# Kernel tuning notes

Measured on AMD Instinct MI355X. Metric: run time of the kernel, lower is better.

## Reference

```python
import jax, jax.numpy as jnp
import numpy as np

B, T, D, H = 32, 4096, 512, 512


def setup_inputs() -> dict:
    key = jax.random.key(0)
    ks = jax.random.split(key, 8)
    s = 1.0 / np.sqrt(D)
    return {
        "hidden_state": jax.random.normal(ks[0], (B, D), jnp.float32),
        "encoder_outputs": jax.random.normal(ks[1], (B, T, D), jnp.float32),
        "W": jax.random.normal(ks[2], (D, H), jnp.float32) * s,
        "U": jax.random.normal(ks[3], (D, H), jnp.float32) * s,
        "V": jax.random.normal(ks[4], (H,), jnp.float32) * s,
        "bias": jnp.zeros((H,), jnp.float32),
        "Wa": jax.random.normal(ks[5], (H, H), jnp.float32) * (1.0 / np.sqrt(H)),
        "ba": jnp.zeros((H,), jnp.float32),
    }


def reference(hidden_state, encoder_outputs, W, U, V, bias, Wa, ba):
    # dens1: [B,1,H] ; dens2: [B,T,H]
    dens1 = jnp.einsum('bd,dh->bh', hidden_state, W)[:, None, :]
    dens2 = jnp.einsum('btd,dh->bth', encoder_outputs, U)
    pre = dens1 + dens2 + bias                       # [B,T,H]
    tanh_ = jnp.tanh(jnp.einsum('bth,hk->btk', pre, Wa) + ba)  # extra Dense(tanh)
    cij = jnp.einsum('bth,h->bt', tanh_, V)          # [B,T]
    alphas = jax.nn.softmax(cij, axis=-1)            # [B,T]
    output = jnp.einsum('btd,bt->bd', encoder_outputs, alphas)  # weighted sum
    return output, alphas
```

## Files before the change

### kernel.cpp

```cpp
#include <hip/hip_runtime.h>
#include <hip/hip_bf16.h>


#define BB 32
#define TT 4096
#define DD 512
#define HH 512

typedef short s16x8 __attribute__((ext_vector_type(8)));
typedef float f32x4 __attribute__((ext_vector_type(4)));

union FU { float f; unsigned u; };

static __device__ __forceinline__ unsigned pack_bf16_trunc(float a, float b) {
    FU ua, ub; ua.f = a; ub.f = b;
    return (ua.u >> 16) | (ub.u & 0xffff0000u);
}

static __device__ __forceinline__ unsigned short f2bf_rne(float x) {
    FU v; v.f = x;
    unsigned u = v.u;
    u = u + 0x7fffu + ((u >> 16) & 1u);
    return (unsigned short)(u >> 16);
}

static __device__ __forceinline__ float tanh_fast(float x) {
    float e = __expf(2.0f * x);
    return 1.0f - 2.0f * __builtin_amdgcn_rcpf(e + 1.0f);
}

__global__ void k_prep(const float* __restrict__ hs, const float* __restrict__ W,
                       const float* __restrict__ bias, const float* __restrict__ Wa,
                       const float* __restrict__ ba, const float* __restrict__ U,
                       float* __restrict__ cvec, unsigned short* __restrict__ Btf) {
    int bi = blockIdx.x;
    int tid = threadIdx.x;
    __shared__ float sm[8 * DD];
    if (bi < 32) {
        int b = bi;
        float* hsb = sm;
        float* gs = sm + DD;
        hsb[tid] = hs[b * DD + tid];
        hsb[tid + 256] = hs[b * DD + tid + 256];
        __syncthreads();
        float a0 = bias[tid], a1 = bias[tid + 256];
        #pragma unroll 4
        for (int d = 0; d < DD; ++d) {
            float h = hsb[d];
            a0 = fmaf(h, W[(size_t)d * HH + tid], a0);
            a1 = fmaf(h, W[(size_t)d * HH + tid + 256], a1);
        }
        gs[tid] = a0;
        gs[tid + 256] = a1;
        __syncthreads();
        float c0 = ba[tid], c1 = ba[tid + 256];
        #pragma unroll 4
        for (int h = 0; h < HH; ++h) {
            float g = gs[h];
            c0 = fmaf(g, Wa[(size_t)h * HH + tid], c0);
            c1 = fmaf(g, Wa[(size_t)h * HH + tid + 256], c1);
        }
        cvec[b * HH + tid] = c0;
        cvec[b * HH + tid + 256] = c1;
    } else {
        int d0 = (bi - 32) * 8;
        float (*Us)[DD] = (float (*)[DD])sm;
        #pragma unroll
        for (int i = 0; i < 16; ++i) {
            int idx = i * 256 + tid;
            Us[idx >> 9][idx & 511] = U[(size_t)(d0 + (idx >> 9)) * HH + (idx & 511)];
        }
        __syncthreads();
        float acc[8][2] = {};
        #pragma unroll 2
        for (int h = 0; h < DD; ++h) {
            float w0 = Wa[(size_t)h * HH + tid];
            float w1 = Wa[(size_t)h * HH + 256 + tid];
            #pragma unroll
            for (int dd = 0; dd < 8; ++dd) {
                float u = Us[dd][h];
                acc[dd][0] = fmaf(u, w0, acc[dd][0]);
                acc[dd][1] = fmaf(u, w1, acc[dd][1]);
            }
        }
        int fk = d0 >> 5, qq = (d0 >> 3) & 3;
        #pragma unroll
        for (int half = 0; half < 2; ++half) {
            int n = tid + half * 256;
            unsigned short tmp[8];
            #pragma unroll
            for (int dd = 0; dd < 8; ++dd) tmp[dd] = f2bf_rne(acc[dd][half]);
            size_t base = ((size_t)((n >> 4) * 16 + fk) * 64 + (n & 15) + (qq << 4)) * 8;
            *(uint4*)&Btf[base] = *(const uint4*)tmp;
        }
    }
}

__global__ void __launch_bounds__(256, 2) k_gemm_tanh(
    const float* __restrict__ e, const unsigned short* __restrict__ Btf,
    const float* __restrict__ cvec, const float* __restrict__ V,
    float* __restrict__ cij) {
    int tid = threadIdx.x;
    int m0 = blockIdx.x * 64;
    int lane = tid & 63, w = tid >> 6;
    int wn = w * 128;
    int lcol = lane & 15, q = lane >> 4;

    __shared__ __align__(16) unsigned short As[64 * DD];

    const float* Abase = e + (size_t)m0 * DD;
    #pragma unroll
    for (int it = 0; it < 16; ++it) {
        int idx = it * 256 + tid;
        int m = idx >> 6, c2 = idx & 63;
        const float* p = Abase + (size_t)m * DD + c2 * 8;
        float4 v0 = *(const float4*)p;
        float4 v1 = *(const float4*)(p + 4);
        uint4 u;
        u.x = pack_bf16_trunc(v0.x, v0.y);
        u.y = pack_bf16_trunc(v0.z, v0.w);
        u.z = pack_bf16_trunc(v1.x, v1.y);
        u.w = pack_bf16_trunc(v1.z, v1.w);
        *(uint4*)&As[(m * 64 + (c2 ^ m)) * 8] = u;
    }
    __syncthreads();

    const unsigned short* Bw = Btf + (size_t)(w * 8) * 16 * 64 * 8;
    f32x4 acc[4][8] = {};
    s16x8 bfr[2][8];
    #pragma unroll
    for (int j = 0; j < 8; ++j)
        bfr[0][j] = *(const s16x8*)(Bw + ((size_t)(j * 16 + 0) * 64 + lane) * 8);

    #pragma unroll
    for (int kk = 0; kk < 16; ++kk) {
        int cur = kk & 1;
        if (kk < 15) {
            #pragma unroll
            for (int j = 0; j < 8; ++j)
                bfr[cur ^ 1][j] =
                    *(const s16x8*)(Bw + ((size_t)(j * 16 + kk + 1) * 64 + lane) * 8);
        }
        s16x8 af[4];
        #pragma unroll
        for (int i = 0; i < 4; ++i) {
            int m = i * 16 + lcol;
            af[i] = *(const s16x8*)&As[(m * 64 + ((kk * 4 + q) ^ m)) * 8];
        }
        #pragma unroll
        for (int i = 0; i < 4; ++i)
            #pragma unroll
            for (int j = 0; j < 8; ++j)
                acc[i][j] = __builtin_amdgcn_mfma_f32_16x16x32_bf16(
                    af[i], bfr[cur][j], acc[i][j], 0, 0, 0);
    }

    __syncthreads();
    float* red = (float*)As;
    int b = m0 >> 12;
    float cvv[8], Vv[8];
    #pragma unroll
    for (int j = 0; j < 8; ++j) {
        int h = wn + j * 16 + lcol;
        cvv[j] = cvec[b * HH + h];
        Vv[j] = V[h];
    }
    #pragma unroll
    for (int i = 0; i < 4; ++i) {
        #pragma unroll
        for (int r = 0; r < 4; ++r) {
            float s = 0.0f;
            #pragma unroll
            for (int j = 0; j < 8; ++j)
                s = fmaf(tanh_fast(acc[i][j][r] + cvv[j]), Vv[j], s);
            s += __shfl_xor(s, 1);
            s += __shfl_xor(s, 2);
            s += __shfl_xor(s, 4);
            s += __shfl_xor(s, 8);
            if (lcol == 0)
                red[w * 64 + i * 16 + q * 4 + r] = s;
        }
    }
    __syncthreads();
    if (tid < 64)
        cij[m0 + tid] = red[tid] + red[64 + tid] + red[128 + tid] + red[192 + tid];
}

__global__ void k_softmax(const float* __restrict__ cij, float* __restrict__ alphas) {
    int b = blockIdx.x, tid = threadIdx.x;
    const float* row = cij + (size_t)b * TT;
    __shared__ float red[4];
    float m = -1e30f;
    for (int t = tid; t < TT; t += 256) m = fmaxf(m, row[t]);
    #pragma unroll
    for (int o = 1; o < 64; o <<= 1) m = fmaxf(m, __shfl_xor(m, o));
    if ((tid & 63) == 0) red[tid >> 6] = m;
    __syncthreads();
    m = fmaxf(fmaxf(red[0], red[1]), fmaxf(red[2], red[3]));
    __syncthreads();
    float sum = 0.0f;
    for (int t = tid; t < TT; t += 256) sum += __expf(row[t] - m);
    #pragma unroll
    for (int o = 1; o < 64; o <<= 1) sum += __shfl_xor(sum, o);
    if ((tid & 63) == 0) red[tid >> 6] = sum;
    __syncthreads();
    float inv = 1.0f / (red[0] + red[1] + red[2] + red[3]);
    for (int t = tid; t < TT; t += 256)
        alphas[(size_t)b * TT + t] = __expf(row[t] - m) * inv;
}

__global__ void k_wsum(const float* __restrict__ e, const float* __restrict__ alphas,
                       float* __restrict__ pw) {
    int b = blockIdx.x >> 6;
    int chunk = blockIdx.x & 63;
    int tid = threadIdx.x;
    int half = tid >> 7, f4 = tid & 127;
    const float* base = e + (size_t)b * TT * DD + (size_t)chunk * 64 * DD + f4 * 4;
    const float* al = alphas + (size_t)b * TT + chunk * 64;
    f32x4 a0 = {0,0,0,0}, a1 = {0,0,0,0}, a2 = {0,0,0,0}, a3 = {0,0,0,0};
    for (int it = 0; it < 8; ++it) {
        int t = it * 8 + half;
        float w0 = al[t], w1 = al[t + 2], w2 = al[t + 4], w3 = al[t + 6];
        a0 += w0 * *(const f32x4*)(base + (size_t)t * DD);
        a1 += w1 * *(const f32x4*)(base + (size_t)(t + 2) * DD);
        a2 += w2 * *(const f32x4*)(base + (size_t)(t + 4) * DD);
        a3 += w3 * *(const f32x4*)(base + (size_t)(t + 6) * DD);
    }
    a0 += a1; a2 += a3; a0 += a2;
    __shared__ f32x4 red[128];
    if (half == 1) red[f4] = a0;
    __syncthreads();
    if (half == 0) {
        a0 += red[f4];
        *(f32x4*)&pw[((size_t)(b * 64 + chunk)) * DD + f4 * 4] = a0;
    }
}

__global__ void k_wred(const float* __restrict__ pw, float* __restrict__ out) {
    int b = blockIdx.x, tid = threadIdx.x;
    float2 acc = {0.0f, 0.0f};
    const float* base = pw + (size_t)b * 64 * DD;
    #pragma unroll 4
    for (int c = 0; c < 64; ++c) {
        float2 v = *(const float2*)(base + (size_t)c * DD + tid * 2);
        acc.x += v.x;
        acc.y += v.y;
    }
    *(float2*)&out[b * DD + tid * 2] = acc;
}

extern "C" void kernel_launch(void* const* d_in, const int* in_sizes, int n_in,
                              void* d_out, int out_size, void* d_ws, size_t ws_size,
                              hipStream_t stream) {
    const float* hs   = (const float*)d_in[0];
    const float* e    = (const float*)d_in[1];
    const float* W    = (const float*)d_in[2];
    const float* U    = (const float*)d_in[3];
    const float* V    = (const float*)d_in[4];
    const float* bias = (const float*)d_in[5];
    const float* Wa   = (const float*)d_in[6];
    const float* ba   = (const float*)d_in[7];

    float* out    = (float*)d_out;
    float* alphas = out + BB * DD;

    float*          cij  = (float*)d_ws;
    float*          cvec = (float*)((char*)d_ws + 524288);
    unsigned short* Btf  = (unsigned short*)((char*)d_ws + 589824);
    float*          pw   = (float*)((char*)d_ws + 1179648);


    k_prep<<<96, 256, 0, stream>>>(hs, W, bias, Wa, ba, U, cvec, Btf);
    k_gemm_tanh<<<2048, 256, 0, stream>>>(e, Btf, cvec, V, cij);
    k_softmax<<<BB, 256, 0, stream>>>(cij, alphas);
    k_wsum<<<BB * 64, 256, 0, stream>>>(e, alphas, pw);
    k_wred<<<BB, 256, 0, stream>>>(pw, out);
}
```

Measured before the change: 574.3 us.

## Split GEMM-tanh across two N-halves with K-staged shared memory and partial scores

The fused GEMM+tanh kernel now launches twice as many blocks, each covering half of the H columns. The A tile is staged through shared memory in two K halves, cutting shared memory and accumulator registers so occupancy can rise (launch bounds 2→3). Each N-half writes its own partial score, and softmax sums the two and caches the exponentials in shared memory so they are not recomputed. In exchange, every encoder row is now read and converted to bf16 twice, and the kernel adds an extra sync and a larger workspace.

```diff
diff --git a/kernel.cpp b/kernel.cpp
--- a/kernel.cpp
+++ b/kernel.cpp
@@ -96,72 +96,76 @@
     }
 }
 
-__global__ void __launch_bounds__(256, 2) k_gemm_tanh(
+__global__ void __launch_bounds__(256, 3) k_gemm_tanh(
     const float* __restrict__ e, const unsigned short* __restrict__ Btf,
     const float* __restrict__ cvec, const float* __restrict__ V,
-    float* __restrict__ cij) {
+    float* __restrict__ cijp) {
     int tid = threadIdx.x;
-    int m0 = blockIdx.x * 64;
+    int nh = blockIdx.x & 1;
+    int m0 = (blockIdx.x >> 1) * 64;
     int lane = tid & 63, w = tid >> 6;
-    int wn = w * 128;
     int lcol = lane & 15, q = lane >> 4;
 
-    __shared__ __align__(16) unsigned short As[64 * DD];
+    __shared__ __align__(16) unsigned short As[64 * 256];
 
     const float* Abase = e + (size_t)m0 * DD;
-    #pragma unroll
-    for (int it = 0; it < 16; ++it) {
-        int idx = it * 256 + tid;
-        int m = idx >> 6, c2 = idx & 63;
-        const float* p = Abase + (size_t)m * DD + c2 * 8;
-        float4 v0 = *(const float4*)p;
-        float4 v1 = *(const float4*)(p + 4);
-        uint4 u;
-        u.x = pack_bf16_trunc(v0.x, v0.y);
-        u.y = pack_bf16_trunc(v0.z, v0.w);
-        u.z = pack_bf16_trunc(v1.x, v1.y);
-        u.w = pack_bf16_trunc(v1.z, v1.w);
-        *(uint4*)&As[(m * 64 + (c2 ^ m)) * 8] = u;
-    }
-    __syncthreads();
-
-    const unsigned short* Bw = Btf + (size_t)(w * 8) * 16 * 64 * 8;
-    f32x4 acc[4][8] = {};
-    s16x8 bfr[2][8];
-    #pragma unroll
-    for (int j = 0; j < 8; ++j)
-        bfr[0][j] = *(const s16x8*)(Bw + ((size_t)(j * 16 + 0) * 64 + lane) * 8);
-
-    #pragma unroll
-    for (int kk = 0; kk < 16; ++kk) {
-        int cur = kk & 1;
-        if (kk < 15) {
-            #pragma unroll
-            for (int j = 0; j < 8; ++j)
-                bfr[cur ^ 1][j] =
-                    *(const s16x8*)(Bw + ((size_t)(j * 16 + kk + 1) * 64 + lane) * 8);
-        }
-        s16x8 af[4];
-        #pragma unroll
-        for (int i = 0; i < 4; ++i) {
-            int m = i * 16 + lcol;
-            af[i] = *(const s16x8*)&As[(m * 64 + ((kk * 4 + q) ^ m)) * 8];
-        }
-        #pragma unroll
-        for (int i = 0; i < 4; ++i)
-            #pragma unroll
-            for (int j = 0; j < 8; ++j)
-                acc[i][j] = __builtin_amdgcn_mfma_f32_16x16x32_bf16(
-                    af[i], bfr[cur][j], acc[i][j], 0, 0, 0);
+    f32x4 acc[4][4] = {};
+    s16x8 bfr[2][4];
+    const unsigned short* Bw = Btf + (size_t)(nh * 16 + w * 4) * 16 * 64 * 8;
+
+    #pragma unroll
+    for (int half = 0; half < 2; ++half) {
+        if (half) __syncthreads();
+        #pragma unroll 2
+        for (int it = 0; it < 8; ++it) {
+            int idx = it * 256 + tid;
+            int m = idx >> 5, c2 = idx & 31;
+            const float* p = Abase + (size_t)m * DD + half * 256 + c2 * 8;
+            float4 v0 = *(const float4*)p;
+            float4 v1 = *(const float4*)(p + 4);
+            uint4 u;
+            u.x = pack_bf16_trunc(v0.x, v0.y);
+            u.y = pack_bf16_trunc(v0.z, v0.w);
+            u.z = pack_bf16_trunc(v1.x, v1.y);
+            u.w = pack_bf16_trunc(v1.z, v1.w);
+            *(uint4*)&As[(m * 32 + (c2 ^ (m & 31))) * 8] = u;
+        }
+        __syncthreads();
+        #pragma unroll
+        for (int j = 0; j < 4; ++j)
+            bfr[0][j] = *(const s16x8*)(Bw +
+                ((size_t)(j * 16 + half * 8) * 64 + lane) * 8);
+        #pragma unroll
+        for (int kk = 0; kk < 8; ++kk) {
+            int cur = kk & 1;
+            if (kk < 7) {
+                #pragma unroll
+                for (int j = 0; j < 4; ++j)
+                    bfr[cur ^ 1][j] = *(const s16x8*)(Bw +
+                        ((size_t)(j * 16 + half * 8 + kk + 1) * 64 + lane) * 8);
+            }
+            s16x8 af[4];
+            #pragma unroll
+            for (int i = 0; i < 4; ++i) {
+                int m = i * 16 + lcol;
+                af[i] = *(const s16x8*)&As[(m * 32 + ((kk * 4 + q) ^ (m & 31))) * 8];
+            }
+            #pragma unroll
+            for (int i = 0; i < 4; ++i)
+                #pragma unroll
+                for (int j = 0; j < 4; ++j)
+                    acc[i][j] = __builtin_amdgcn_mfma_f32_16x16x32_bf16(
+                        af[i], bfr[cur][j], acc[i][j], 0, 0, 0);
+        }
     }
 
     __syncthreads();
     float* red = (float*)As;
     int b = m0 >> 12;
-    float cvv[8], Vv[8];
-    #pragma unroll
-    for (int j = 0; j < 8; ++j) {
-        int h = wn + j * 16 + lcol;
+    float cvv[4], Vv[4];
+    #pragma unroll
+    for (int j = 0; j < 4; ++j) {
+        int h = nh * 256 + w * 64 + j * 16 + lcol;
         cvv[j] = cvec[b * HH + h];
         Vv[j] = V[h];
     }
@@ -171,7 +175,7 @@
         for (int r = 0; r < 4; ++r) {
             float s = 0.0f;
             #pragma unroll
-            for (int j = 0; j < 8; ++j)
+            for (int j = 0; j < 4; ++j)
                 s = fmaf(tanh_fast(acc[i][j][r] + cvv[j]), Vv[j], s);
             s += __shfl_xor(s, 1);
             s += __shfl_xor(s, 2);
@@ -183,15 +187,18 @@
     }
     __syncthreads();
     if (tid < 64)
-        cij[m0 + tid] = red[tid] + red[64 + tid] + red[128 + tid] + red[192 + tid];
-}
-
-__global__ void k_softmax(const float* __restrict__ cij, float* __restrict__ alphas) {
+        cijp[(size_t)nh * (BB * TT) + m0 + tid] =
+            red[tid] + red[64 + tid] + red[128 + tid] + red[192 + tid];
+}
+
+__global__ void k_softmax(const float* __restrict__ cijp, float* __restrict__ alphas) {
     int b = blockIdx.x, tid = threadIdx.x;
-    const float* row = cij + (size_t)b * TT;
+    const float* r0 = cijp + (size_t)b * TT;
+    const float* r1 = r0 + (size_t)BB * TT;
     __shared__ float red[4];
+    __shared__ float rowbuf[TT / 256 * 256];
     float m = -1e30f;
-    for (int t = tid; t < TT; t += 256) m = fmaxf(m, row[t]);
+    for (int t = tid; t < TT; t += 256) m = fmaxf(m, r0[t] + r1[t]);
     #pragma unroll
     for (int o = 1; o < 64; o <<= 1) m = fmaxf(m, __shfl_xor(m, o));
     if ((tid & 63) == 0) red[tid >> 6] = m;
@@ -199,14 +206,18 @@
     m = fmaxf(fmaxf(red[0], red[1]), fmaxf(red[2], red[3]));
     __syncthreads();
     float sum = 0.0f;
-    for (int t = tid; t < TT; t += 256) sum += __expf(row[t] - m);
+    for (int t = tid; t < TT; t += 256) {
+        float v = __expf(r0[t] + r1[t] - m);
+        rowbuf[t & 4095] = v;
+        sum += v;
+    }
     #pragma unroll
     for (int o = 1; o < 64; o <<= 1) sum += __shfl_xor(sum, o);
     if ((tid & 63) == 0) red[tid >> 6] = sum;
     __syncthreads();
     float inv = 1.0f / (red[0] + red[1] + red[2] + red[3]);
     for (int t = tid; t < TT; t += 256)
-        alphas[(size_t)b * TT + t] = __expf(row[t] - m) * inv;
+        alphas[(size_t)b * TT + t] = rowbuf[t] * inv;
 }
 
 __global__ void k_wsum(const float* __restrict__ e, const float* __restrict__ alphas,
@@ -264,15 +275,15 @@
     float* out    = (float*)d_out;
     float* alphas = out + BB * DD;
 
-    float*          cij  = (float*)d_ws;
-    float*          cvec = (float*)((char*)d_ws + 524288);
-    unsigned short* Btf  = (unsigned short*)((char*)d_ws + 589824);
-    float*          pw   = (float*)((char*)d_ws + 1179648);
+    float*          cijp = (float*)d_ws;
+    float*          cvec = (float*)((char*)d_ws + 1048576);
+    unsigned short* Btf  = (unsigned short*)((char*)d_ws + 1114112);
+    float*          pw   = (float*)((char*)d_ws + 1703936);
 
 
     k_prep<<<96, 256, 0, stream>>>(hs, W, bias, Wa, ba, U, cvec, Btf);
-    k_gemm_tanh<<<2048, 256, 0, stream>>>(e, Btf, cvec, V, cij);
-    k_softmax<<<BB, 256, 0, stream>>>(cij, alphas);
+    k_gemm_tanh<<<4096, 256, 0, stream>>>(e, Btf, cvec, V, cijp);
+    k_softmax<<<BB, 256, 0, stream>>>(cijp, alphas);
     k_wsum<<<BB * 64, 256, 0, stream>>>(e, alphas, pw);
     k_wred<<<BB, 256, 0, stream>>>(pw, out);
 }
```

New measurement: 577.9 us. About the same (+0.6%).

## Shrink GEMM M-tile to 32 rows with 8 waves, cache softmax exps in LDS

Applied to the files above, without the earlier changes.

The fused GEMM+tanh kernel now handles 32 rows per block with 512 threads (8 waves, each owning 64 output columns), halving per-wave accumulators and LDS so more blocks fit per CU. The A-tile swizzle is reworked for the smaller tile, and the cross-wave reduction is extended to sum 8 partials. Softmax stores exp values in shared memory so they are not recomputed, and the weighted-sum loop gets an unroll hint. The trade-off is that each B fragment loaded from global/L2 is reused across half as many rows, which doubles total B traffic.

```diff
diff --git a/kernel.cpp b/kernel.cpp
--- a/kernel.cpp
+++ b/kernel.cpp
@@ -96,22 +96,21 @@
     }
 }
 
-__global__ void __launch_bounds__(256, 2) k_gemm_tanh(
+__global__ void __launch_bounds__(512, 4) k_gemm_tanh(
     const float* __restrict__ e, const unsigned short* __restrict__ Btf,
     const float* __restrict__ cvec, const float* __restrict__ V,
     float* __restrict__ cij) {
     int tid = threadIdx.x;
-    int m0 = blockIdx.x * 64;
+    int m0 = blockIdx.x * 32;
     int lane = tid & 63, w = tid >> 6;
-    int wn = w * 128;
     int lcol = lane & 15, q = lane >> 4;
 
-    __shared__ __align__(16) unsigned short As[64 * DD];
+    __shared__ __align__(16) unsigned short As[32 * 512];
 
     const float* Abase = e + (size_t)m0 * DD;
     #pragma unroll
-    for (int it = 0; it < 16; ++it) {
-        int idx = it * 256 + tid;
+    for (int it = 0; it < 4; ++it) {
+        int idx = it * 512 + tid;
         int m = idx >> 6, c2 = idx & 63;
         const float* p = Abase + (size_t)m * DD + c2 * 8;
         float4 v0 = *(const float4*)p;
@@ -121,36 +120,38 @@
         u.y = pack_bf16_trunc(v0.z, v0.w);
         u.z = pack_bf16_trunc(v1.x, v1.y);
         u.w = pack_bf16_trunc(v1.z, v1.w);
-        *(uint4*)&As[(m * 64 + (c2 ^ m)) * 8] = u;
-    }
-    __syncthreads();
-
-    const unsigned short* Bw = Btf + (size_t)(w * 8) * 16 * 64 * 8;
-    f32x4 acc[4][8] = {};
-    s16x8 bfr[2][8];
-    #pragma unroll
-    for (int j = 0; j < 8; ++j)
-        bfr[0][j] = *(const s16x8*)(Bw + ((size_t)(j * 16 + 0) * 64 + lane) * 8);
+        *(uint4*)&As[(m * 64 + (c2 >> 5) * 32 + ((c2 & 31) ^ (m & 31))) * 8] = u;
+    }
+    __syncthreads();
+
+    const unsigned short* Bw = Btf + (size_t)(w * 4) * 16 * 64 * 8;
+    f32x4 acc[2][4] = {};
+    s16x8 bfr[2][4];
+    #pragma unroll
+    for (int j = 0; j < 4; ++j)
+        bfr[0][j] = *(const s16x8*)(Bw + ((size_t)(j * 16) * 64 + lane) * 8);
 
     #pragma unroll
     for (int kk = 0; kk < 16; ++kk) {
         int cur = kk & 1;
         if (kk < 15) {
             #pragma unroll
-            for (int j = 0; j < 8; ++j)
-                bfr[cur ^ 1][j] =
-                    *(const s16x8*)(Bw + ((size_t)(j * 16 + kk + 1) * 64 + lane) * 8);
-        }
-        s16x8 af[4];
-        #pragma unroll
-        for (int i = 0; i < 4; ++i) {
+            for (int j = 0; j < 4; ++j)
+                bfr[cur ^ 1][j] = *(const s16x8*)(Bw +
+                    ((size_t)(j * 16 + kk + 1) * 64 + lane) * 8);
+        }
+        s16x8 af[2];
+        #pragma unroll
+        for (int i = 0; i < 2; ++i) {
             int m = i * 16 + lcol;
-            af[i] = *(const s16x8*)&As[(m * 64 + ((kk * 4 + q) ^ m)) * 8];
-        }
-        #pragma unroll
-        for (int i = 0; i < 4; ++i)
-            #pragma unroll
-            for (int j = 0; j < 8; ++j)
+            int c2 = kk * 4 + q;
+            af[i] = *(const s16x8*)&As[
+                (m * 64 + (c2 >> 5) * 32 + ((c2 & 31) ^ (m & 31))) * 8];
+        }
+        #pragma unroll
+        for (int i = 0; i < 2; ++i)
+            #pragma unroll
+            for (int j = 0; j < 4; ++j)
                 acc[i][j] = __builtin_amdgcn_mfma_f32_16x16x32_bf16(
                     af[i], bfr[cur][j], acc[i][j], 0, 0, 0);
     }
@@ -158,38 +159,43 @@
     __syncthreads();
     float* red = (float*)As;
     int b = m0 >> 12;
-    float cvv[8], Vv[8];
-    #pragma unroll
-    for (int j = 0; j < 8; ++j) {
-        int h = wn + j * 16 + lcol;
+    float cvv[4], Vv[4];
+    #pragma unroll
+    for (int j = 0; j < 4; ++j) {
+        int h = w * 64 + j * 16 + lcol;
         cvv[j] = cvec[b * HH + h];
         Vv[j] = V[h];
     }
     #pragma unroll
-    for (int i = 0; i < 4; ++i) {
+    for (int i = 0; i < 2; ++i) {
         #pragma unroll
         for (int r = 0; r < 4; ++r) {
             float s = 0.0f;
             #pragma unroll
-            for (int j = 0; j < 8; ++j)
+            for (int j = 0; j < 4; ++j)
                 s = fmaf(tanh_fast(acc[i][j][r] + cvv[j]), Vv[j], s);
             s += __shfl_xor(s, 1);
             s += __shfl_xor(s, 2);
             s += __shfl_xor(s, 4);
             s += __shfl_xor(s, 8);
             if (lcol == 0)
-                red[w * 64 + i * 16 + q * 4 + r] = s;
-        }
-    }
-    __syncthreads();
-    if (tid < 64)
-        cij[m0 + tid] = red[tid] + red[64 + tid] + red[128 + tid] + red[192 + tid];
+                red[w * 32 + i * 16 + q * 4 + r] = s;
+        }
+    }
+    __syncthreads();
+    if (tid < 32) {
+        float s = 0.0f;
+        #pragma unroll
+        for (int ww = 0; ww < 8; ++ww) s += red[ww * 32 + tid];
+        cij[m0 + tid] = s;
+    }
 }
 
 __global__ void k_softmax(const float* __restrict__ cij, float* __restrict__ alphas) {
     int b = blockIdx.x, tid = threadIdx.x;
     const float* row = cij + (size_t)b * TT;
     __shared__ float red[4];
+    __shared__ float rowbuf[TT];
     float m = -1e30f;
     for (int t = tid; t < TT; t += 256) m = fmaxf(m, row[t]);
     #pragma unroll
@@ -199,14 +205,18 @@
     m = fmaxf(fmaxf(red[0], red[1]), fmaxf(red[2], red[3]));
     __syncthreads();
     float sum = 0.0f;
-    for (int t = tid; t < TT; t += 256) sum += __expf(row[t] - m);
+    for (int t = tid; t < TT; t += 256) {
+        float v = __expf(row[t] - m);
+        rowbuf[t] = v;
+        sum += v;
+    }
     #pragma unroll
     for (int o = 1; o < 64; o <<= 1) sum += __shfl_xor(sum, o);
     if ((tid & 63) == 0) red[tid >> 6] = sum;
     __syncthreads();
     float inv = 1.0f / (red[0] + red[1] + red[2] + red[3]);
     for (int t = tid; t < TT; t += 256)
-        alphas[(size_t)b * TT + t] = __expf(row[t] - m) * inv;
+        alphas[(size_t)b * TT + t] = rowbuf[t] * inv;
 }
 
 __global__ void k_wsum(const float* __restrict__ e, const float* __restrict__ alphas,
@@ -218,6 +228,7 @@
     const float* base = e + (size_t)b * TT * DD + (size_t)chunk * 64 * DD + f4 * 4;
     const float* al = alphas + (size_t)b * TT + chunk * 64;
     f32x4 a0 = {0,0,0,0}, a1 = {0,0,0,0}, a2 = {0,0,0,0}, a3 = {0,0,0,0};
+    #pragma unroll 2
     for (int it = 0; it < 8; ++it) {
         int t = it * 8 + half;
         float w0 = al[t], w1 = al[t + 2], w2 = al[t + 4], w3 = al[t + 6];
@@ -271,7 +282,7 @@
 
 
     k_prep<<<96, 256, 0, stream>>>(hs, W, bias, Wa, ba, U, cvec, Btf);
-    k_gemm_tanh<<<2048, 256, 0, stream>>>(e, Btf, cvec, V, cij);
+    k_gemm_tanh<<<4096, 512, 0, stream>>>(e, Btf, cvec, V, cij);
     k_softmax<<<BB, 256, 0, stream>>>(cij, alphas);
     k_wsum<<<BB * 64, 256, 0, stream>>>(e, alphas, pw);
     k_wred<<<BB, 256, 0, stream>>>(pw, out);
```

Result: no change. 575.8 us (+0.3%).
